# Kernel optimization log

Hardware: AMD Instinct MI355X
Metric: run time of the kernel (lower is better)

## Reference

```python
import jax, jax.numpy as jnp
import numpy as np

RATIOS = (0.5, 1.0, 2.0)
SCALES = (8.0, 16.0, 32.0)
FEAT_STRIDE = 16
BASE_SIZE = 16.0
NMS_THRESH = 0.7
N_PRE = 6000   # pre-NMS top-k (eval-mode ProposalCreator default)
N_POST = 300   # post-NMS proposals per image (eval-mode default)
MIN_SIZE = 16.0
SCALE = 1.0


def generate_anchor_base():
    ab = np.zeros((len(RATIOS) * len(SCALES), 4), np.float32)
    for i, r in enumerate(RATIOS):
        for j, s in enumerate(SCALES):
            h = BASE_SIZE * s * np.sqrt(r)
            w = BASE_SIZE * s * np.sqrt(1.0 / r)
            ab[i * len(SCALES) + j] = [-h / 2.0, -w / 2.0, h / 2.0, w / 2.0]
    return jnp.asarray(ab)


def enumerate_shifted_anchor(anchor_base, feat_stride, H, W):
    sy = jnp.arange(H, dtype=jnp.float32) * feat_stride
    sx = jnp.arange(W, dtype=jnp.float32) * feat_stride
    sx, sy = jnp.meshgrid(sx, sy)  # row-major over (y, x), matching torch permute order
    shift = jnp.stack([sy.ravel(), sx.ravel(), sy.ravel(), sx.ravel()], axis=1)  # [K,4]
    anchors = anchor_base[None, :, :] + shift[:, None, :]  # [K, A, 4]
    return anchors.reshape(-1, 4)


def loc2bbox(anchor, loc):
    # boxes in (y1, x1, y2, x2) format
    h = anchor[:, 2] - anchor[:, 0]
    w = anchor[:, 3] - anchor[:, 1]
    cy = anchor[:, 0] + 0.5 * h
    cx = anchor[:, 1] + 0.5 * w
    dy, dx, dh, dw = loc[:, 0], loc[:, 1], loc[:, 2], loc[:, 3]
    cy = cy + dy * h
    cx = cx + dx * w
    h = h * jnp.exp(dh)
    w = w * jnp.exp(dw)
    return jnp.stack([cy - 0.5 * h, cx - 0.5 * w, cy + 0.5 * h, cx + 0.5 * w], axis=1)


def nms_fixed(boxes, scores):
    # boxes [N_PRE,4] sorted desc by scores; greedy NMS emitting N_POST picks (padded)
    area = (boxes[:, 2] - boxes[:, 0]) * (boxes[:, 3] - boxes[:, 1])

    def step(sc, _):
        i = jnp.argmax(sc)
        v = sc[i] > -jnp.inf
        b = boxes[i]
        yy1 = jnp.maximum(boxes[:, 0], b[0])
        xx1 = jnp.maximum(boxes[:, 1], b[1])
        yy2 = jnp.minimum(boxes[:, 2], b[2])
        xx2 = jnp.minimum(boxes[:, 3], b[3])
        inter = jnp.maximum(yy2 - yy1, 0.0) * jnp.maximum(xx2 - xx1, 0.0)
        iou = inter / (area + area[i] - inter + 1e-9)
        sc = jnp.where((iou > NMS_THRESH) & v, -jnp.inf, sc)
        sc = sc.at[i].set(-jnp.inf)
        return sc, (i, v)

    _, (idx, valid) = jax.lax.scan(step, scores, None, length=N_POST)
    return jnp.where(valid[:, None], boxes[idx], 0.0)  # [N_POST, 4]


def proposal_one(loc, score, anchor, img_h, img_w):
    roi = loc2bbox(anchor, loc)
    roi = jnp.stack([
        jnp.clip(roi[:, 0], 0.0, img_h), jnp.clip(roi[:, 1], 0.0, img_w),
        jnp.clip(roi[:, 2], 0.0, img_h), jnp.clip(roi[:, 3], 0.0, img_w)], axis=1)
    hs = roi[:, 2] - roi[:, 0]
    ws = roi[:, 3] - roi[:, 1]
    min_size = MIN_SIZE * SCALE
    valid = (hs >= min_size) & (ws >= min_size)
    s = jnp.where(valid, score, -jnp.inf)
    top_s, top_i = jax.lax.top_k(s, N_PRE)
    return nms_fixed(roi[top_i], top_s)


def setup_inputs() -> dict:
    key = jax.random.key(0)
    ks = jax.random.split(key, 4)
    B, C, H, W = 8, 512, 64, 64
    A = 9
    return {
        "x": jax.random.normal(ks[0], (B, C, H, W), jnp.float32),
        "conv_w": jax.random.normal(ks[1], (C, C, 3, 3), jnp.float32) * 0.01,
        "conv_b": jnp.zeros((C,), jnp.float32),
        "loc_w": jax.random.normal(ks[2], (A * 4, C, 1, 1), jnp.float32) * 0.01,
        "loc_b": jnp.zeros((A * 4,), jnp.float32),
        "cls_w": jax.random.normal(ks[3], (A * 2, C, 1, 1), jnp.float32) * 0.01,
        "cls_b": jnp.zeros((A * 2,), jnp.float32),
        "img_h": 1024,
        "img_w": 1024,
    }


def reference(x, conv_w, conv_b, loc_w, loc_b, cls_w, cls_b, img_h, img_w):
    dn = ("NCHW", "OIHW", "NCHW")
    h = jax.lax.conv_general_dilated(x, conv_w, (1, 1), "SAME", dimension_numbers=dn)
    h = jax.nn.relu(h + conv_b[None, :, None, None])
    cls = jax.nn.sigmoid(
        jax.lax.conv_general_dilated(h, cls_w, (1, 1), "VALID", dimension_numbers=dn)
        + cls_b[None, :, None, None])
    loc = (jax.lax.conv_general_dilated(h, loc_w, (1, 1), "VALID", dimension_numbers=dn)
           + loc_b[None, :, None, None])
    B, _, H, W = h.shape
    anchor = enumerate_shifted_anchor(generate_anchor_base(), FEAT_STRIDE, H, W)
    pred_locations = loc.transpose(0, 2, 3, 1).reshape(B, -1, 4)          # [B, HWA, 4]
    cls_hw = cls.transpose(0, 2, 3, 1)                                     # [B, H, W, 2A]
    objectness = cls_hw.reshape(B, H, W, -1, 2)[..., 1].reshape(B, -1)     # [B, HWA]
    pred_cls_scores = cls_hw.reshape(B, -1, 2)                             # [B, HWA, 2]
    fh = jnp.float32(img_h)
    fw = jnp.float32(img_w)
    rois = jax.vmap(lambda l, s: proposal_one(l, s, anchor, fh, fw))(pred_locations, objectness)
    rois = rois.reshape(B * N_POST, 4)
    roi_indices = jnp.repeat(jnp.arange(B, dtype=jnp.int64 if jax.config.jax_enable_x64 else jnp.int32), N_POST)
    return pred_cls_scores, pred_locations, rois, roi_indices
```

## Files before the change

kernel.cpp:

```cpp
#include <hip/hip_runtime.h>
#include <cstdint>
#include <cmath>


#define AS1U(p) ((const __attribute__((address_space(1))) unsigned int*)(p))
#define AS3U(p) ((__attribute__((address_space(3))) unsigned int*)(p))

typedef float f32x2 __attribute__((ext_vector_type(2)));
typedef float f32x4 __attribute__((ext_vector_type(4)));

__global__ __launch_bounds__(512) void k_wtrans(
        const float* __restrict__ w, float* __restrict__ wT) {
    const int cik = blockIdx.x;
    const int co = threadIdx.x;
    wT[(size_t)cik * 512 + co] = w[(size_t)co * 4608 + cik];
}

__global__ __launch_bounds__(256) void k_conv3x3_pk(
        const float* __restrict__ x, const float* __restrict__ wT,
        const float* __restrict__ bias, const float* __restrict__ zeropad,
        float* __restrict__ hout) {
    __shared__ __align__(16) float xs[8][6][68];
    __shared__ __align__(16) float wl[8][9][68];

    const int ytile = blockIdx.x;
    const int co0 = blockIdx.y * 64;
    const int b = blockIdx.z;
    const int t = threadIdx.x;
    const int xq = t & 7;
    const int coq = (t >> 3) & 7;
    const int yy = t >> 6;
    const int lane = t & 63;
    const int y0 = ytile * 4;

    if (t < 48) { int ci = t / 6, ry = t % 6; xs[ci][ry][0] = 0.f; xs[ci][ry][65] = 0.f; }

    f32x2 acc2[4][8];
#pragma unroll
    for (int c = 0; c < 4; ++c)
#pragma unroll
        for (int i = 0; i < 8; ++i) acc2[c][i] = (f32x2){0.f, 0.f};

    const int gy0 = y0 - 1;
    const float* xb = x + ((size_t)b * 512) * 4096;

    for (int ci0 = 0; ci0 < 512; ci0 += 8) {
        __syncthreads();
#pragma unroll
        for (int j = 0; j < 12; ++j) {
            const int ci = 2 * yy + (j >= 6 ? 1 : 0);
            const int ry = (j >= 6) ? (j - 6) : j;
            const int gy = gy0 + ry;
            const float* src = (gy >= 0 && gy < 64)
                ? xb + ((size_t)(ci0 + ci) * 64 + gy) * 64 + lane
                : zeropad + lane;
            __builtin_amdgcn_global_load_lds(AS1U(src), AS3U(&xs[ci][ry][1]), 4, 0, 0);
        }
#pragma unroll
        for (int c2 = 0; c2 < 2; ++c2) {
            const int cil = 2 * yy + c2;
#pragma unroll
            for (int k = 0; k < 9; ++k) {
                const float* src = wT + ((size_t)(ci0 + cil) * 9 + k) * 512 + co0 + lane;
                __builtin_amdgcn_global_load_lds(AS1U(src), AS3U(&wl[cil][k][0]), 4, 0, 0);
            }
        }
        __syncthreads();
#pragma unroll
        for (int ci = 0; ci < 8; ++ci) {
#pragma unroll
            for (int ky = 0; ky < 3; ++ky) {
                const float* xr = &xs[ci][yy + ky][xq * 8];
                const f32x4 a0 = *(const f32x4*)(xr);
                const f32x4 a1 = *(const f32x4*)(xr + 4);
                const f32x2 a2 = *(const f32x2*)(xr + 8);
                f32x2 xw2[10];
                xw2[0] = (f32x2){a0[0], a0[0]}; xw2[1] = (f32x2){a0[1], a0[1]};
                xw2[2] = (f32x2){a0[2], a0[2]}; xw2[3] = (f32x2){a0[3], a0[3]};
                xw2[4] = (f32x2){a1[0], a1[0]}; xw2[5] = (f32x2){a1[1], a1[1]};
                xw2[6] = (f32x2){a1[2], a1[2]}; xw2[7] = (f32x2){a1[3], a1[3]};
                xw2[8] = (f32x2){a2[0], a2[0]}; xw2[9] = (f32x2){a2[1], a2[1]};
#pragma unroll
                for (int kx = 0; kx < 3; ++kx) {
                    const f32x4 w0 = *(const f32x4*)&wl[ci][ky * 3 + kx][coq * 8];
                    const f32x4 w1 = *(const f32x4*)&wl[ci][ky * 3 + kx][coq * 8 + 4];
                    const f32x2 w00 = (f32x2){w0[0], w0[1]};
                    const f32x2 w01 = (f32x2){w0[2], w0[3]};
                    const f32x2 w10 = (f32x2){w1[0], w1[1]};
                    const f32x2 w11 = (f32x2){w1[2], w1[3]};
#pragma unroll
                    for (int i = 0; i < 8; ++i) {
                        const f32x2 xv2 = xw2[i + kx];
                        acc2[0][i] = __builtin_elementwise_fma(w00, xv2, acc2[0][i]);
                        acc2[1][i] = __builtin_elementwise_fma(w01, xv2, acc2[1][i]);
                        acc2[2][i] = __builtin_elementwise_fma(w10, xv2, acc2[2][i]);
                        acc2[3][i] = __builtin_elementwise_fma(w11, xv2, acc2[3][i]);
                    }
                }
            }
        }
    }
    const int y = y0 + yy;
#pragma unroll
    for (int c = 0; c < 8; ++c) {
        const int co = co0 + coq * 8 + c;
        const float bv = bias[co];
        float* op = hout + (((size_t)b * 512 + co) * 64 + y) * 64 + xq * 8;
        float4 o0, o1;
        o0.x = fmaxf(acc2[c >> 1][0][c & 1] + bv, 0.f);
        o0.y = fmaxf(acc2[c >> 1][1][c & 1] + bv, 0.f);
        o0.z = fmaxf(acc2[c >> 1][2][c & 1] + bv, 0.f);
        o0.w = fmaxf(acc2[c >> 1][3][c & 1] + bv, 0.f);
        o1.x = fmaxf(acc2[c >> 1][4][c & 1] + bv, 0.f);
        o1.y = fmaxf(acc2[c >> 1][5][c & 1] + bv, 0.f);
        o1.z = fmaxf(acc2[c >> 1][6][c & 1] + bv, 0.f);
        o1.w = fmaxf(acc2[c >> 1][7][c & 1] + bv, 0.f);
        *(float4*)(op) = o0;
        *(float4*)(op + 4) = o1;
    }
}

__global__ __launch_bounds__(256) void k_conv3x3(
        const float* __restrict__ x, const float* __restrict__ w,
        const float* __restrict__ bias, const float* __restrict__ zeropad,
        float* __restrict__ hout) {
    __shared__ __align__(16) float xs[8][6][68];
    __shared__ __align__(16) float wl[8][9][68];
    const int ytile = blockIdx.x;
    const int co0 = blockIdx.y * 64;
    const int b = blockIdx.z;
    const int t = threadIdx.x;
    const int xq = t & 7;
    const int coq = (t >> 3) & 7;
    const int yy = t >> 6;
    const int lane = t & 63;
    const int y0 = ytile * 4;
    if (t < 48) { int ci = t / 6, ry = t % 6; xs[ci][ry][0] = 0.f; xs[ci][ry][65] = 0.f; }
    float acc[8][8];
#pragma unroll
    for (int c = 0; c < 8; ++c)
#pragma unroll
        for (int i = 0; i < 8; ++i) acc[c][i] = 0.f;
    const int co_s = t >> 2, qs = t & 3;
    const float* wsrc = w + (size_t)(co0 + co_s) * 4608 + qs * 18;
    float* wrow = &wl[0][0][0] + (size_t)(2 * qs) * 9 * 68 + co_s;
    const int gy0 = y0 - 1;
    const float* xb = x + ((size_t)b * 512) * 4096;
    for (int ci0 = 0; ci0 < 512; ci0 += 8) {
        __syncthreads();
#pragma unroll
        for (int j = 0; j < 12; ++j) {
            const int ci = 2 * yy + (j >= 6 ? 1 : 0);
            const int ry = (j >= 6) ? (j - 6) : j;
            const int gy = gy0 + ry;
            const float* src = (gy >= 0 && gy < 64)
                ? xb + ((size_t)(ci0 + ci) * 64 + gy) * 64 + lane
                : zeropad + lane;
            __builtin_amdgcn_global_load_lds(AS1U(src), AS3U(&xs[ci][ry][1]), 4, 0, 0);
        }
        {
            const float2* wp2 = (const float2*)(wsrc + (size_t)ci0 * 9);
#pragma unroll
            for (int j2 = 0; j2 < 9; ++j2) {
                float2 f = wp2[j2];
                const int i0 = 2 * j2, i1 = 2 * j2 + 1;
                wrow[(i0 < 9 ? 0 : 9 * 68) + (i0 < 9 ? i0 : i0 - 9) * 68] = f.x;
                wrow[(i1 < 9 ? 0 : 9 * 68) + (i1 < 9 ? i1 : i1 - 9) * 68] = f.y;
            }
        }
        __syncthreads();
#pragma unroll
        for (int ci = 0; ci < 8; ++ci) {
#pragma unroll
            for (int ky = 0; ky < 3; ++ky) {
                const float* xr = &xs[ci][yy + ky][xq * 8];
                const float4 a0 = *(const float4*)(xr);
                const float4 a1 = *(const float4*)(xr + 4);
                const float2 a2 = *(const float2*)(xr + 8);
                float xw[10];
                xw[0] = a0.x; xw[1] = a0.y; xw[2] = a0.z; xw[3] = a0.w;
                xw[4] = a1.x; xw[5] = a1.y; xw[6] = a1.z; xw[7] = a1.w;
                xw[8] = a2.x; xw[9] = a2.y;
#pragma unroll
                for (int kx = 0; kx < 3; ++kx) {
                    const float4 w0 = *(const float4*)&wl[ci][ky * 3 + kx][coq * 8];
                    const float4 w1 = *(const float4*)&wl[ci][ky * 3 + kx][coq * 8 + 4];
#pragma unroll
                    for (int i = 0; i < 8; ++i) {
                        const float xv = xw[i + kx];
                        acc[0][i] += w0.x * xv; acc[1][i] += w0.y * xv;
                        acc[2][i] += w0.z * xv; acc[3][i] += w0.w * xv;
                        acc[4][i] += w1.x * xv; acc[5][i] += w1.y * xv;
                        acc[6][i] += w1.z * xv; acc[7][i] += w1.w * xv;
                    }
                }
            }
        }
    }
    const int y = y0 + yy;
#pragma unroll
    for (int c = 0; c < 8; ++c) {
        const int co = co0 + coq * 8 + c;
        const float bv = bias[co];
        float* op = hout + (((size_t)b * 512 + co) * 64 + y) * 64 + xq * 8;
        float4 o0, o1;
        o0.x = fmaxf(acc[c][0] + bv, 0.f); o0.y = fmaxf(acc[c][1] + bv, 0.f);
        o0.z = fmaxf(acc[c][2] + bv, 0.f); o0.w = fmaxf(acc[c][3] + bv, 0.f);
        o1.x = fmaxf(acc[c][4] + bv, 0.f); o1.y = fmaxf(acc[c][5] + bv, 0.f);
        o1.z = fmaxf(acc[c][6] + bv, 0.f); o1.w = fmaxf(acc[c][7] + bv, 0.f);
        *(float4*)(op) = o0;
        *(float4*)(op + 4) = o1;
    }
}

__global__ __launch_bounds__(256) void k_head(
        const float* __restrict__ h,
        const float* __restrict__ cls_w, const float* __restrict__ cls_b,
        const float* __restrict__ loc_w, const float* __restrict__ loc_b,
        const int* __restrict__ img_h_p, const int* __restrict__ img_w_p,
        float* __restrict__ out_cls, float* __restrict__ out_loc,
        float* __restrict__ boxes, float* __restrict__ scores) {
    __shared__ float wC[18][128];
    __shared__ float wO[36][128];
    const int t = threadIdx.x;
    const int tg = blockIdx.x * 256 + t;
    const int b = tg >> 12;
    const int pos = tg & 4095;
    const int y = pos >> 6, xc = pos & 63;
    float accC[18], accL[36];
#pragma unroll
    for (int o = 0; o < 18; ++o) accC[o] = 0.f;
#pragma unroll
    for (int o = 0; o < 36; ++o) accL[o] = 0.f;
    const float* hp = h + (size_t)b * 2097152 + pos;
    for (int c4 = 0; c4 < 4; ++c4) {
        const int ci0 = c4 * 128;
        __syncthreads();
#pragma unroll
        for (int j = 0; j < 27; ++j) {
            const int idx = t + j * 256;
            const int o = idx >> 7, cc = idx & 127;
            if (o < 18) wC[o][cc] = cls_w[o * 512 + ci0 + cc];
            else        wO[o - 18][cc] = loc_w[(o - 18) * 512 + ci0 + cc];
        }
        __syncthreads();
#pragma unroll 4
        for (int cc = 0; cc < 128; ++cc) {
            const float hv = hp[(size_t)(ci0 + cc) * 4096];
#pragma unroll
            for (int o = 0; o < 18; ++o) accC[o] += wC[o][cc] * hv;
#pragma unroll
            for (int o = 0; o < 36; ++o) accL[o] += wO[o][cc] * hv;
        }
    }
    const float fh = (float)(*img_h_p);
    const float fw = (float)(*img_w_p);
    {
        const size_t obase = (size_t)b * 73728 + (size_t)pos * 18;
#pragma unroll
        for (int o = 0; o < 18; ++o) {
            accC[o] += cls_b[o];
            out_cls[obase + o] = 1.f / (1.f + expf(-accC[o]));
        }
    }
    {
        const size_t lbase = (size_t)b * 147456 + (size_t)pos * 36;
#pragma unroll
        for (int o = 0; o < 36; ++o) {
            accL[o] += loc_b[o];
            out_loc[lbase + o] = accL[o];
        }
    }
    const float sy = (float)(y * 16), sx = (float)(xc * 16);
    const double RR[3] = {0.5, 1.0, 2.0};
    const double SS[3] = {8.0, 16.0, 32.0};
#pragma unroll
    for (int a = 0; a < 9; ++a) {
        const double r = RR[a / 3], s = SS[a % 3];
        const double hd = 16.0 * s * sqrt(r);
        const double wd = 16.0 * s * sqrt(1.0 / r);
        const float ab0 = (float)(-hd / 2.0), ab1 = (float)(-wd / 2.0);
        const float ab2 = (float)(hd / 2.0), ab3 = (float)(wd / 2.0);
        const float a0 = ab0 + sy, a1 = ab1 + sx, a2 = ab2 + sy, a3 = ab3 + sx;
        float hh = a2 - a0, ww = a3 - a1;
        float cy = a0 + 0.5f * hh, cx = a1 + 0.5f * ww;
        const float dy = accL[a * 4 + 0], dx = accL[a * 4 + 1];
        const float dh = accL[a * 4 + 2], dw = accL[a * 4 + 3];
        cy = cy + dy * hh;
        cx = cx + dx * ww;
        hh = hh * expf(dh);
        ww = ww * expf(dw);
        float y1 = cy - 0.5f * hh, x1 = cx - 0.5f * ww;
        float y2 = cy + 0.5f * hh, x2 = cx + 0.5f * ww;
        y1 = fminf(fmaxf(y1, 0.f), fh); x1 = fminf(fmaxf(x1, 0.f), fw);
        y2 = fminf(fmaxf(y2, 0.f), fh); x2 = fminf(fmaxf(x2, 0.f), fw);
        const bool valid = ((y2 - y1) >= 16.f) && ((x2 - x1) >= 16.f);
        const float sc = 1.f / (1.f + expf(-accC[a * 2 + 1]));
        const int n = pos * 9 + a;
        float* bp = boxes + ((size_t)b * 36864 + n) * 4;
        bp[0] = y1; bp[1] = x1; bp[2] = y2; bp[3] = x2;
        scores[(size_t)b * 36864 + n] = valid ? sc : -INFINITY;
    }
}

__device__ __forceinline__ unsigned fmap(float f) {
    unsigned bits = __float_as_uint(f);
    return ((int)bits < 0) ? ~bits : (bits | 0x80000000u);
}

__global__ __launch_bounds__(1024) void k_select(
        const float* __restrict__ scores, unsigned* __restrict__ sel) {
    __shared__ unsigned h2[16][256];
    __shared__ unsigned hist[256];
    __shared__ unsigned tieL[1024];
    __shared__ unsigned sh_pref, sh_k, sh_cg, sh_ct;
    const int b = blockIdx.x;
    const int t = threadIdx.x;
    const int lane = t & 63;
    const int wid = t >> 6;
    const unsigned long long lmlt = (1ull << lane) - 1ull;
    const float* sp = scores + (size_t)b * 36864;
    unsigned pref = 0;
    unsigned k = 6000;
    for (int p = 3; p >= 0; --p) {
        for (int z = t; z < 4096; z += 1024) ((unsigned*)h2)[z] = 0;
        __syncthreads();
        const int sh = p * 8;
        for (int i4 = t * 4; i4 < 36864; i4 += 4096) {
            const float4 v = *(const float4*)(sp + i4);
            const float vv[4] = {v.x, v.y, v.z, v.w};
#pragma unroll
            for (int e = 0; e < 4; ++e) {
                unsigned u = fmap(vv[e]);
                bool match = (p == 3) || ((u >> (sh + 8)) == (pref >> (sh + 8)));
                if (match) atomicAdd(&h2[wid][(u >> sh) & 255u], 1u);
            }
        }
        __syncthreads();
        if (t < 256) {
            unsigned s = 0;
#pragma unroll
            for (int j = 0; j < 16; ++j) s += h2[j][t];
            hist[t] = s;
        }
        __syncthreads();
        if (t == 0) {
            unsigned c = 0;
            int bsel = 0;
            for (int bin = 255; bin >= 0; --bin) {
                unsigned c2 = c + hist[bin];
                if (c2 >= k) { bsel = bin; k = k - c; break; }
                c = c2;
            }
            pref |= ((unsigned)bsel) << sh;
            sh_pref = pref; sh_k = k;
        }
        __syncthreads();
        pref = sh_pref; k = sh_k;
        __syncthreads();
    }
    if (t == 0) { sh_cg = 0; sh_ct = 0; }
    __syncthreads();
    const unsigned uthr = pref;
    for (int i4 = t * 4; i4 < 36864; i4 += 4096) {
        const float4 v = *(const float4*)(sp + i4);
        const float vv[4] = {v.x, v.y, v.z, v.w};
#pragma unroll
        for (int e = 0; e < 4; ++e) {
            const int i = i4 + e;
            unsigned u = fmap(vv[e]);
            const bool g = (u > uthr);
            const bool eq = (u == uthr);
            unsigned long long bg = __ballot(g);
            if (bg) {
                int lead = __ffsll((unsigned long long)bg) - 1;
                unsigned basev = 0;
                if (lane == lead) basev = atomicAdd(&sh_cg, (unsigned)__popcll(bg));
                basev = __shfl(basev, lead, 64);
                if (g) sel[(size_t)b * 6000 + basev + (unsigned)__popcll(bg & lmlt)] = (unsigned)i;
            }
            unsigned long long be = __ballot(eq);
            if (be) {
                int lead = __ffsll((unsigned long long)be) - 1;
                unsigned baset = 0;
                if (lane == lead) baset = atomicAdd(&sh_ct, (unsigned)__popcll(be));
                baset = __shfl(baset, lead, 64);
                if (eq) {
                    unsigned tp = baset + (unsigned)__popcll(be & lmlt);
                    if (tp < 1024) tieL[tp] = (unsigned)i;
                }
            }
        }
    }
    __syncthreads();
    const unsigned G = sh_cg;
    const unsigned T = sh_ct;
    const unsigned need = k;
    const unsigned Tc = T < 1024u ? T : 1024u;
    if ((unsigned)t >= Tc) tieL[t] = 0xFFFFFFFFu;
    __syncthreads();
    if (need > 0) {
        if (T > 1) {
            for (int kk = 2; kk <= 1024; kk <<= 1) {
                for (int j = kk >> 1; j > 0; j >>= 1) {
                    int ixj = t ^ j;
                    if (ixj > t) {
                        unsigned va = tieL[t], vb = tieL[ixj];
                        bool up = ((t & kk) == 0);
                        if (up ? (va > vb) : (va < vb)) { tieL[t] = vb; tieL[ixj] = va; }
                    }
                    __syncthreads();
                }
            }
        }
        if ((unsigned)t < need) sel[(size_t)b * 6000 + G + t] = tieL[t];
    }
}

__global__ __launch_bounds__(1024) void k_nms(
        const float* __restrict__ boxes, const float* __restrict__ scores,
        const unsigned* __restrict__ sel,
        float* __restrict__ rois, float* __restrict__ roi_idx) {
    __shared__ unsigned long long warr[2][16];
    __shared__ float wbox[2][16][4];
    const int b = blockIdx.x;
    const int t = threadIdx.x;
    const unsigned UNEG = 0x007FFFFFu;
    float bx[6][4];
    unsigned long long key[6];
#pragma unroll
    for (int j = 0; j < 6; ++j) {
        int s = t + j * 1024;
        if (s < 6000) {
            unsigned idx = sel[(size_t)b * 6000 + s];
            const float* bp = boxes + ((size_t)b * 36864 + idx) * 4;
            bx[j][0] = bp[0]; bx[j][1] = bp[1]; bx[j][2] = bp[2]; bx[j][3] = bp[3];
            unsigned u = fmap(scores[(size_t)b * 36864 + idx]);
            key[j] = ((unsigned long long)u << 32) | (unsigned)(~idx);
        } else {
            key[j] = 0ull;
            bx[j][0] = bx[j][1] = bx[j][2] = bx[j][3] = 0.f;
        }
    }
    const int lane = t & 63;
    const int wid = t >> 6;
    float* orow = rois + (size_t)b * 300 * 4;
    for (int k = 0; k < 300; ++k) {
        const int pb = k & 1;
        unsigned long long m = key[0];
        float b0 = bx[0][0], b1 = bx[0][1], b2 = bx[0][2], b3 = bx[0][3];
#pragma unroll
        for (int j = 1; j < 6; ++j) {
            if (key[j] > m) { m = key[j]; b0 = bx[j][0]; b1 = bx[j][1]; b2 = bx[j][2]; b3 = bx[j][3]; }
        }
        const unsigned long long lm = m;
#pragma unroll
        for (int d = 32; d > 0; d >>= 1) {
            unsigned long long o = __shfl_xor(m, d, 64);
            if (o > m) m = o;
        }
        unsigned long long own = __ballot(lm == m);
        if (lane == __ffsll(own) - 1) {
            warr[pb][wid] = m;
            wbox[pb][wid][0] = b0; wbox[pb][wid][1] = b1;
            wbox[pb][wid][2] = b2; wbox[pb][wid][3] = b3;
        }
        __syncthreads();
        unsigned long long wk = warr[pb][0];
        int wm = 0;
#pragma unroll
        for (int i = 1; i < 16; ++i) {
            unsigned long long v = warr[pb][i];
            if (v > wk) { wk = v; wm = i; }
        }
        const unsigned uhi = (unsigned)(wk >> 32);
        if (uhi > UNEG) {
            const float py1 = wbox[pb][wm][0], px1 = wbox[pb][wm][1];
            const float py2 = wbox[pb][wm][2], px2 = wbox[pb][wm][3];
            const float parea = (py2 - py1) * (px2 - px1);
            if (t == 0) {
                orow[k * 4 + 0] = py1; orow[k * 4 + 1] = px1;
                orow[k * 4 + 2] = py2; orow[k * 4 + 3] = px2;
                roi_idx[b * 300 + k] = (float)b;
            }
#pragma unroll
            for (int j = 0; j < 6; ++j) {
                if ((unsigned)(key[j] >> 32) > UNEG) {
                    float yy1 = fmaxf(bx[j][0], py1);
                    float xx1 = fmaxf(bx[j][1], px1);
                    float yy2 = fminf(bx[j][2], py2);
                    float xx2 = fminf(bx[j][3], px2);
                    float inter = fmaxf(yy2 - yy1, 0.f) * fmaxf(xx2 - xx1, 0.f);
                    float area = (bx[j][2] - bx[j][0]) * (bx[j][3] - bx[j][1]);
                    float iou = inter / (area + parea - inter + 1e-9f);
                    if (iou > 0.7f)
                        key[j] = ((unsigned long long)UNEG << 32) | (key[j] & 0xFFFFFFFFull);
                }
            }
        } else {
            if (t == 0) {
                orow[k * 4 + 0] = 0.f; orow[k * 4 + 1] = 0.f;
                orow[k * 4 + 2] = 0.f; orow[k * 4 + 3] = 0.f;
                roi_idx[b * 300 + k] = (float)b;
            }
        }
    }
}

extern "C" void kernel_launch(void* const* d_in, const int* in_sizes, int n_in,
                              void* d_out, int out_size, void* d_ws, size_t ws_size,
                              hipStream_t stream) {
    (void)in_sizes; (void)n_in; (void)out_size;
    const float* x      = (const float*)d_in[0];
    const float* conv_w = (const float*)d_in[1];
    const float* conv_b = (const float*)d_in[2];
    const float* loc_w  = (const float*)d_in[3];
    const float* loc_b  = (const float*)d_in[4];
    const float* cls_w  = (const float*)d_in[5];
    const float* cls_b  = (const float*)d_in[6];
    const int* img_h    = (const int*)d_in[7];
    const int* img_w    = (const int*)d_in[8];

    char* ws = (char*)d_ws;
    float*    h      = (float*)(ws + 0);
    float*    boxes  = (float*)(ws + 67108864);
    float*    scores = (float*)(ws + 71827456);
    unsigned* sel    = (unsigned*)(ws + 73007104);
    float*    zp     = (float*)(ws + 73199104);
    float*    wT     = (float*)(ws + 73199360);

    float* out      = (float*)d_out;
    float* out_cls  = out;
    float* out_loc  = out + 589824;
    float* rois     = out + 1769472;
    float* ridx     = out + 1779072;

    const bool big_ws = (ws_size >= 82636544ull);

    hipMemsetAsync(zp, 0, 256, stream);
    if (big_ws) {
        k_wtrans<<<dim3(4608), 512, 0, stream>>>(conv_w, wT);
        k_conv3x3_pk<<<dim3(16, 8, 8), 256, 0, stream>>>(x, wT, conv_b, zp, h);
    } else {
        k_conv3x3<<<dim3(16, 8, 8), 256, 0, stream>>>(x, conv_w, conv_b, zp, h);
    }
    k_head<<<dim3(128), 256, 0, stream>>>(h, cls_w, cls_b, loc_w, loc_b,
                                          img_h, img_w, out_cls, out_loc, boxes, scores);
    k_select<<<dim3(8), 1024, 0, stream>>>(scores, sel);
    k_nms<<<dim3(8), 1024, 0, stream>>>(boxes, scores, sel, rois, ridx);
}
```

Baseline: 2.906 ms.

## Tile weight transpose, widen conv channel chunk, pack head FMAs with more blocks

Replaces the strided per-element weight transpose with a 64x64 shared-memory tiled transpose so both reads and writes are coalesced. Doubles the conv input-channel chunk per barrier from 8 to 16, which halves the number of sync/load phases at the cost of twice the LDS use per block. Reworks the 1x1 head kernel to keep weights in a position-major LDS layout read as float4 and accumulated with packed 2-wide FMAs. It also launches 256 blocks of 128 threads instead of 128 blocks of 256 to spread the head across more CUs.

```diff
diff --git a/kernel.cpp b/kernel.cpp
--- a/kernel.cpp
+++ b/kernel.cpp
@@ -9,19 +9,33 @@
 typedef float f32x2 __attribute__((ext_vector_type(2)));
 typedef float f32x4 __attribute__((ext_vector_type(4)));
 
-__global__ __launch_bounds__(512) void k_wtrans(
+__global__ __launch_bounds__(256) void k_wtrans_t(
         const float* __restrict__ w, float* __restrict__ wT) {
-    const int cik = blockIdx.x;
-    const int co = threadIdx.x;
-    wT[(size_t)cik * 512 + co] = w[(size_t)co * 4608 + cik];
+    __shared__ float tile[64][65];
+    const int cik0 = blockIdx.x * 64;
+    const int co0 = blockIdx.y * 64;
+    const int t = threadIdx.x;
+    const int l = t & 63;
+    const int r = t >> 6;
+#pragma unroll
+    for (int it = 0; it < 16; ++it) {
+        const int co_l = r + 4 * it;
+        tile[l][co_l] = w[(size_t)(co0 + co_l) * 4608 + cik0 + l];
+    }
+    __syncthreads();
+#pragma unroll
+    for (int it = 0; it < 16; ++it) {
+        const int cik_l = r + 4 * it;
+        wT[(size_t)(cik0 + cik_l) * 512 + co0 + l] = tile[cik_l][l];
+    }
 }
 
 __global__ __launch_bounds__(256) void k_conv3x3_pk(
         const float* __restrict__ x, const float* __restrict__ wT,
         const float* __restrict__ bias, const float* __restrict__ zeropad,
         float* __restrict__ hout) {
-    __shared__ __align__(16) float xs[8][6][68];
-    __shared__ __align__(16) float wl[8][9][68];
+    __shared__ __align__(16) float xs[16][6][68];
+    __shared__ __align__(16) float wl[16][9][68];
 
     const int ytile = blockIdx.x;
     const int co0 = blockIdx.y * 64;
@@ -33,7 +47,7 @@
     const int lane = t & 63;
     const int y0 = ytile * 4;
 
-    if (t < 48) { int ci = t / 6, ry = t % 6; xs[ci][ry][0] = 0.f; xs[ci][ry][65] = 0.f; }
+    if (t < 96) { int ci = t / 6, ry = t % 6; xs[ci][ry][0] = 0.f; xs[ci][ry][65] = 0.f; }
 
     f32x2 acc2[4][8];
 #pragma unroll
@@ -44,12 +58,12 @@
     const int gy0 = y0 - 1;
     const float* xb = x + ((size_t)b * 512) * 4096;
 
-    for (int ci0 = 0; ci0 < 512; ci0 += 8) {
-        __syncthreads();
-#pragma unroll
-        for (int j = 0; j < 12; ++j) {
-            const int ci = 2 * yy + (j >= 6 ? 1 : 0);
-            const int ry = (j >= 6) ? (j - 6) : j;
+    for (int ci0 = 0; ci0 < 512; ci0 += 16) {
+        __syncthreads();
+#pragma unroll
+        for (int j = 0; j < 24; ++j) {
+            const int ci = 4 * yy + (j / 6);
+            const int ry = j % 6;
             const int gy = gy0 + ry;
             const float* src = (gy >= 0 && gy < 64)
                 ? xb + ((size_t)(ci0 + ci) * 64 + gy) * 64 + lane
@@ -57,8 +71,8 @@
             __builtin_amdgcn_global_load_lds(AS1U(src), AS3U(&xs[ci][ry][1]), 4, 0, 0);
         }
 #pragma unroll
-        for (int c2 = 0; c2 < 2; ++c2) {
-            const int cil = 2 * yy + c2;
+        for (int c2 = 0; c2 < 4; ++c2) {
+            const int cil = 4 * yy + c2;
 #pragma unroll
             for (int k = 0; k < 9; ++k) {
                 const float* src = wT + ((size_t)(ci0 + cil) * 9 + k) * 512 + co0 + lane;
@@ -67,7 +81,7 @@
         }
         __syncthreads();
 #pragma unroll
-        for (int ci = 0; ci < 8; ++ci) {
+        for (int ci = 0; ci < 16; ++ci) {
 #pragma unroll
             for (int ky = 0; ky < 3; ++ky) {
                 const float* xr = &xs[ci][yy + ky][xq * 8];
@@ -213,46 +227,52 @@
     }
 }
 
-__global__ __launch_bounds__(256) void k_head(
+__global__ __launch_bounds__(128) void k_head(
         const float* __restrict__ h,
         const float* __restrict__ cls_w, const float* __restrict__ cls_b,
         const float* __restrict__ loc_w, const float* __restrict__ loc_b,
         const int* __restrict__ img_h_p, const int* __restrict__ img_w_p,
         float* __restrict__ out_cls, float* __restrict__ out_loc,
         float* __restrict__ boxes, float* __restrict__ scores) {
-    __shared__ float wC[18][128];
-    __shared__ float wO[36][128];
+    __shared__ __align__(16) float wAll[128][60];
     const int t = threadIdx.x;
-    const int tg = blockIdx.x * 256 + t;
+    const int tg = blockIdx.x * 128 + t;
     const int b = tg >> 12;
     const int pos = tg & 4095;
     const int y = pos >> 6, xc = pos & 63;
-    float accC[18], accL[36];
-#pragma unroll
-    for (int o = 0; o < 18; ++o) accC[o] = 0.f;
-#pragma unroll
-    for (int o = 0; o < 36; ++o) accL[o] = 0.f;
+    f32x2 acc2[27];
+#pragma unroll
+    for (int p = 0; p < 27; ++p) acc2[p] = (f32x2){0.f, 0.f};
     const float* hp = h + (size_t)b * 2097152 + pos;
     for (int c4 = 0; c4 < 4; ++c4) {
         const int ci0 = c4 * 128;
         __syncthreads();
 #pragma unroll
-        for (int j = 0; j < 27; ++j) {
-            const int idx = t + j * 256;
-            const int o = idx >> 7, cc = idx & 127;
-            if (o < 18) wC[o][cc] = cls_w[o * 512 + ci0 + cc];
-            else        wO[o - 18][cc] = loc_w[(o - 18) * 512 + ci0 + cc];
+        for (int j = 0; j < 54; ++j) {
+            wAll[t][j] = (j < 18) ? cls_w[j * 512 + ci0 + t]
+                                  : loc_w[(j - 18) * 512 + ci0 + t];
         }
         __syncthreads();
 #pragma unroll 4
         for (int cc = 0; cc < 128; ++cc) {
             const float hv = hp[(size_t)(ci0 + cc) * 4096];
-#pragma unroll
-            for (int o = 0; o < 18; ++o) accC[o] += wC[o][cc] * hv;
-#pragma unroll
-            for (int o = 0; o < 36; ++o) accL[o] += wO[o][cc] * hv;
-        }
-    }
+            const f32x2 hv2 = (f32x2){hv, hv};
+            const float* wr = &wAll[cc][0];
+#pragma unroll
+            for (int q = 0; q < 13; ++q) {
+                const f32x4 w4 = *(const f32x4*)(wr + 4 * q);
+                acc2[2 * q]     = __builtin_elementwise_fma((f32x2){w4[0], w4[1]}, hv2, acc2[2 * q]);
+                acc2[2 * q + 1] = __builtin_elementwise_fma((f32x2){w4[2], w4[3]}, hv2, acc2[2 * q + 1]);
+            }
+            const f32x2 wtl = *(const f32x2*)(wr + 52);
+            acc2[26] = __builtin_elementwise_fma(wtl, hv2, acc2[26]);
+        }
+    }
+    float accC[18], accL[36];
+#pragma unroll
+    for (int o = 0; o < 18; ++o) accC[o] = acc2[o >> 1][o & 1];
+#pragma unroll
+    for (int l = 0; l < 36; ++l) accL[l] = acc2[9 + (l >> 1)][l & 1];
     const float fh = (float)(*img_h_p);
     const float fw = (float)(*img_w_p);
     {
@@ -539,12 +559,12 @@
 
     hipMemsetAsync(zp, 0, 256, stream);
     if (big_ws) {
-        k_wtrans<<<dim3(4608), 512, 0, stream>>>(conv_w, wT);
+        k_wtrans_t<<<dim3(72, 8), 256, 0, stream>>>(conv_w, wT);
         k_conv3x3_pk<<<dim3(16, 8, 8), 256, 0, stream>>>(x, wT, conv_b, zp, h);
     } else {
         k_conv3x3<<<dim3(16, 8, 8), 256, 0, stream>>>(x, conv_w, conv_b, zp, h);
     }
-    k_head<<<dim3(128), 256, 0, stream>>>(h, cls_w, cls_b, loc_w, loc_b,
+    k_head<<<dim3(256), 128, 0, stream>>>(h, cls_w, cls_b, loc_w, loc_b,
                                           img_h, img_w, out_cls, out_loc, boxes, scores);
     k_select<<<dim3(8), 1024, 0, stream>>>(scores, sel);
     k_nms<<<dim3(8), 1024, 0, stream>>>(boxes, scores, sel, rois, ridx);
```

Result: no change. 2.906 ms (+0.0%).
